# Performance work log

Hardware: AMD Instinct MI355X
Metric: run time of the kernel (lower is better)

The kernel has to match this reference:

```python
import jax, jax.numpy as jnp
import numpy as np

B, S, D, H = 2, 2048, 1024, 16
DK = D // H


def setup_inputs() -> dict:
    key = jax.random.key(0)
    ks = jax.random.split(key, 11)
    scale = 1.0 / np.sqrt(D)
    inp = {
        "k": jax.random.normal(ks[0], (B, S, D), jnp.float32),
        "q": jax.random.normal(ks[1], (B, S, D), jnp.float32),
        "v": jax.random.normal(ks[2], (B, S, D), jnp.float32),
        "w_q": jax.random.normal(ks[3], (D, D), jnp.float32) * scale,
        "b_q": jax.random.normal(ks[4], (D,), jnp.float32) * 0.01,
        "w_k": jax.random.normal(ks[5], (D, D), jnp.float32) * scale,
        "b_k": jax.random.normal(ks[6], (D,), jnp.float32) * 0.01,
        "w_v": jax.random.normal(ks[7], (D, D), jnp.float32) * scale,
        "b_v": jax.random.normal(ks[8], (D,), jnp.float32) * 0.01,
        "w_o": jax.random.normal(ks[9], (D, D), jnp.float32) * scale,
        "b_o": jax.random.normal(ks[10], (D,), jnp.float32) * 0.01,
        # causal mask; positions with mask==0 get -1e9 (masked_fill semantics)
        "mask": jnp.tril(jnp.ones((1, 1, S, S), jnp.int32)),
    }
    return inp


def reference(k, q, v, w_q, b_q, w_k, b_k, w_v, b_v, w_o, b_o, mask):
    MINUS_INF = -1000000000.0

    def proj(x, w, b):
        # nn.Linear: x @ w.T + b, then split heads -> [B, H, S, DK]
        y = x @ w.T + b
        return y.reshape(B, S, H, DK).transpose(0, 2, 1, 3)

    Q = proj(q, w_q, b_q)
    K = proj(k, w_k, b_k)
    V = proj(v, w_v, b_v)

    # [B, H, Sq, Sk] scores
    scores = jnp.einsum("bhqd,bhkd->bhqk", Q, K) / jnp.sqrt(jnp.float32(DK))
    scores = jnp.where(mask == 0, MINUS_INF, scores)
    attn = jax.nn.softmax(scores, axis=-1)

    out = jnp.einsum("bhqk,bhkd->bhqd", attn, V)  # [B, H, S, DK]
    out = out.transpose(0, 2, 1, 3).reshape(B, S, D)  # concat heads
    return out @ w_o.T + b_o
```

## Files before the change

kernel.cpp:

```cpp
#include <hip/hip_runtime.h>

typedef __bf16 bf16;
typedef __bf16 v8bf __attribute__((ext_vector_type(8)));
typedef __bf16 v4bf __attribute__((ext_vector_type(4)));
typedef float  v4f  __attribute__((ext_vector_type(4)));

#define MFMA16(a,b,c) __builtin_amdgcn_mfma_f32_16x16x32_bf16((a),(b),(c),0,0,0)

static constexpr int Sq = 2048;
static constexpr size_t NI = 4194304;
static constexpr size_t NW = 1048576;

__device__ __forceinline__ void gld_lds16(const void* g, void* l) {
  __builtin_amdgcn_global_load_lds(
      (__attribute__((address_space(1))) unsigned int*)g,
      (__attribute__((address_space(3))) unsigned int*)l,
      16, 0, 0);
}

__device__ __forceinline__ float exp2_raw(float x) {
  return __builtin_amdgcn_exp2f(x);
}

__global__ __launch_bounds__(256) void convert_kernel(
    const float* __restrict__ q, const float* __restrict__ k, const float* __restrict__ v,
    const float* __restrict__ wq, const float* __restrict__ wk,
    const float* __restrict__ wv, const float* __restrict__ wo,
    bf16* __restrict__ dst)
{
  const int NI4 = 1048576;
  const int NW4 = 262144;
  int idx = blockIdx.x * 256 + threadIdx.x;
  const float* src; size_t dstoff; int local;
  if (idx < 3 * NI4) {
    int a = idx >> 20; local = idx & (NI4 - 1);
    src = (a == 0) ? q : ((a == 1) ? k : v);
    dstoff = (size_t)a * NI;
  } else {
    int t = idx - 3 * NI4;
    int a = t >> 18; local = t & (NW4 - 1);
    src = (a == 0) ? wq : ((a == 1) ? wk : ((a == 2) ? wv : wo));
    dstoff = 3 * NI + (size_t)a * NW;
  }
  float4 f = ((const float4*)src)[local];
  v4bf hv = { (bf16)f.x, (bf16)f.y, (bf16)f.z, (bf16)f.w };
  *(v4bf*)(dst + dstoff + (size_t)local * 4) = hv;
}

__device__ __forceinline__ void gemm_bt_body(
    const bf16* __restrict__ A, const bf16* __restrict__ Bw,
    const float* __restrict__ bias, bf16* __restrict__ outh,
    float* __restrict__ outf, int bm, int bn, int mode)
{
  __shared__ alignas(16) bf16 As[128 * 32];
  __shared__ alignas(16) bf16 Bs[128 * 32];
  const int tid = threadIdx.x;
  const int wave = tid >> 6, lane = tid & 63;
  const int quad = lane >> 4, l15 = lane & 15;
  const int wm = (wave >> 1) * 64, wn = (wave & 1) * 64;
  const int lrow = lane >> 2, lcol = (lane & 3) * 8;

  v4f acc[4][4];
#pragma unroll
  for (int i = 0; i < 4; i++)
#pragma unroll
    for (int j = 0; j < 4; j++) { v4f z = {0.f, 0.f, 0.f, 0.f}; acc[i][j] = z; }

  const bf16* gA = A  + (size_t)(bm + wave * 32 + lrow) * 1024 + lcol;
  const bf16* gB = Bw + (size_t)(bn + wave * 32 + lrow) * 1024 + lcol;
  bf16* lA0 = &As[(wave * 32) * 32];
  bf16* lA1 = &As[(wave * 32 + 16) * 32];
  bf16* lB0 = &Bs[(wave * 32) * 32];
  bf16* lB1 = &Bs[(wave * 32 + 16) * 32];

  for (int k0 = 0; k0 < 1024; k0 += 32) {
    gld_lds16(gA + k0, lA0);
    gld_lds16(gA + 16 * 1024 + k0, lA1);
    gld_lds16(gB + k0, lB0);
    gld_lds16(gB + 16 * 1024 + k0, lB1);
    __syncthreads();
    v8bf af[4], bfr[4];
#pragma unroll
    for (int i = 0; i < 4; i++)
      af[i] = *(const v8bf*)&As[(wm + i * 16 + l15) * 32 + quad * 8];
#pragma unroll
    for (int j = 0; j < 4; j++)
      bfr[j] = *(const v8bf*)&Bs[(wn + j * 16 + l15) * 32 + quad * 8];
#pragma unroll
    for (int i = 0; i < 4; i++)
#pragma unroll
      for (int j = 0; j < 4; j++)
        acc[i][j] = MFMA16(af[i], bfr[j], acc[i][j]);
    __syncthreads();
  }

#pragma unroll
  for (int i = 0; i < 4; i++) {
    const int m0 = bm + wm + i * 16 + quad * 4;
#pragma unroll
    for (int j = 0; j < 4; j++) {
      const int n = bn + wn + j * 16 + l15;
      const float bv = bias[n];
      if (mode == 1) {
#pragma unroll
        for (int r = 0; r < 4; r++)
          outf[(size_t)(m0 + r) * 1024 + n] = acc[i][j][r] + bv;
      } else if (mode == 2) {
        int b_ = m0 >> 11, s_ = m0 & 2047;
        int h_ = n >> 6,  dk = n & 63;
        v4bf pk;
#pragma unroll
        for (int r = 0; r < 4; r++) pk[r] = (bf16)(acc[i][j][r] + bv);
        *(v4bf*)&outh[((size_t)((b_ * 16 + h_) * 64 + dk)) * 2048 + s_] = pk;
      } else {
        const float sc = (mode == 3) ? 0.18033688011112042f : 1.0f;
        int h_ = n >> 6,  dk = n & 63;
#pragma unroll
        for (int r = 0; r < 4; r++) {
          int m = m0 + r;
          int b_ = m >> 11, s_ = m & 2047;
          outh[(((size_t)(b_ * 16 + h_) * 2048 + s_) << 6) + dk] =
              (bf16)((acc[i][j][r] + bv) * sc);
        }
      }
    }
  }
}

__global__ __launch_bounds__(256, 2) void gemm_proj_kernel(
    const bf16* qb, const bf16* kb, const bf16* vb,
    const bf16* wqb, const bf16* wkb, const bf16* wvb,
    const float* bq, const float* bk, const float* bv,
    bf16* Qh, bf16* Kh, bf16* VhT)
{
  const bf16* A; const bf16* W; const float* bias; bf16* out; int mode;
  if (blockIdx.z == 0)      { A = qb; W = wqb; bias = bq; out = Qh;  mode = 3; }
  else if (blockIdx.z == 1) { A = kb; W = wkb; bias = bk; out = Kh;  mode = 0; }
  else                      { A = vb; W = wvb; bias = bv; out = VhT; mode = 2; }
  gemm_bt_body(A, W, bias, out, nullptr, blockIdx.y * 128, blockIdx.x * 128, mode);
}

__global__ __launch_bounds__(256, 2) void gemm_final_kernel(
    const bf16* Ob, const bf16* wob, const float* bo, float* out)
{
  gemm_bt_body(Ob, wob, bo, nullptr, out, blockIdx.y * 128, blockIdx.x * 128, 1);
}

__global__ __launch_bounds__(128, 2) void attn_kernel(
    const bf16* __restrict__ Qh, const bf16* __restrict__ Kh,
    const bf16* __restrict__ VhT, bf16* __restrict__ Ob)
{
  __shared__ alignas(16) bf16 Ps[2][32 * 72];
  const int tid = threadIdx.x;
  const int wave = tid >> 6, lane = tid & 63;
  const int quad = lane >> 4, l15 = lane & 15;
  const int bh = blockIdx.x, gy = blockIdx.y;
  const int b = bh >> 4, h = bh & 15;
  const int r8 = gy & 7, q8 = gy >> 3;
  const int u = 8 * q8 + ((q8 & 1) ? (7 - r8) : r8);
  const int qt = 2 * u + wave;
  const int L = u;
  const bf16* Qb = Qh + (size_t)bh * Sq * 64;
  const bf16* Kb = Kh + (size_t)bh * Sq * 64;
  const bf16* Vb = VhT + (size_t)bh * 64 * Sq;
  bf16* Pw = &Ps[wave][0];
  const int r0 = qt * 32;

  v8bf aq[2][2];
#pragma unroll
  for (int s = 0; s < 2; s++)
#pragma unroll
    for (int ks = 0; ks < 2; ks++)
      aq[s][ks] = *(const v8bf*)&Qb[(size_t)(r0 + s * 16 + l15) * 64 + ks * 32 + quad * 8];

  float lsum[2][4];
  v4f o[2][4];
#pragma unroll
  for (int s = 0; s < 2; s++)
#pragma unroll
    for (int r = 0; r < 4; r++) lsum[s][r] = 0.f;
#pragma unroll
  for (int s = 0; s < 2; s++)
#pragma unroll
    for (int j = 0; j < 4; j++) { v4f z = {0.f, 0.f, 0.f, 0.f}; o[s][j] = z; }

  auto loadK = [&](int kb, v8bf (&BK)[4][2]) {
#pragma unroll
    for (int n = 0; n < 4; n++) {
      BK[n][0] = *(const v8bf*)&Kb[(size_t)(kb + n * 16 + l15) * 64 + quad * 8];
      BK[n][1] = *(const v8bf*)&Kb[(size_t)(kb + n * 16 + l15) * 64 + 32 + quad * 8];
    }
  };
  auto loadV = [&](int kb, v8bf (&BV)[4][2]) {
#pragma unroll
    for (int n = 0; n < 4; n++) {
      BV[n][0] = *(const v8bf*)&Vb[(size_t)(n * 16 + l15) * 2048 + kb + quad * 8];
      BV[n][1] = *(const v8bf*)&Vb[(size_t)(n * 16 + l15) * 2048 + kb + 32 + quad * 8];
    }
  };
  auto compute = [&](const v8bf (&BK)[4][2], const v8bf (&BV)[4][2], int kc, bool diag) {
    const int kbase = kc * 64;
#pragma unroll
    for (int s = 0; s < 2; s++) {
      v4f cn[4];
#pragma unroll
      for (int n = 0; n < 4; n++) {
        v4f z = {0.f, 0.f, 0.f, 0.f};
        cn[n] = MFMA16(aq[s][0], BK[n][0], z);
        cn[n] = MFMA16(aq[s][1], BK[n][1], cn[n]);
      }
      const int rbase = r0 + s * 16 + quad * 4;
#pragma unroll
      for (int n = 0; n < 4; n++) {
        const int colg = kbase + n * 16 + l15;
#pragma unroll
        for (int r = 0; r < 4; r++) {
          float e = exp2_raw(cn[n][r]);
          if (diag && colg > rbase + r) e = 0.f;
          lsum[s][r] += e;
          Pw[(s * 16 + quad * 4 + r) * 72 + n * 16 + l15] = (bf16)e;
        }
      }
    }
#pragma unroll
    for (int s = 0; s < 2; s++) {
      v8bf ap0 = *(const v8bf*)&Pw[(s * 16 + l15) * 72 + quad * 8];
      v8bf ap1 = *(const v8bf*)&Pw[(s * 16 + l15) * 72 + 32 + quad * 8];
#pragma unroll
      for (int j = 0; j < 4; j++) {
        o[s][j] = MFMA16(ap0, BV[j][0], o[s][j]);
        o[s][j] = MFMA16(ap1, BV[j][1], o[s][j]);
      }
    }
  };

  v8bf bk0[4][2], bk1[4][2], bvv[4][2];
  loadK(0, bk0);
  int kc = 0;
  while (kc < L) {
    loadV(kc * 64, bvv);
    loadK((kc + 1) * 64, bk1);
    compute(bk0, bvv, kc, false);
    ++kc;
    if (kc >= L) {
      loadV(kc * 64, bvv);
      compute(bk1, bvv, kc, true);
      kc = -1;
      break;
    }
    loadV(kc * 64, bvv);
    loadK((kc + 1) * 64, bk0);
    compute(bk1, bvv, kc, false);
    ++kc;
  }
  if (kc >= 0) {
    loadV(kc * 64, bvv);
    compute(bk0, bvv, kc, true);
  }

#pragma unroll
  for (int s = 0; s < 2; s++)
#pragma unroll
    for (int r = 0; r < 4; r++) {
#pragma unroll
      for (int off = 1; off < 16; off <<= 1)
        lsum[s][r] += __shfl_xor(lsum[s][r], off, 64);
    }
#pragma unroll
  for (int s = 0; s < 2; s++)
#pragma unroll
    for (int r = 0; r < 4; r++) {
      const float inv = 1.0f / lsum[s][r];
      const int sg = r0 + s * 16 + quad * 4 + r;
#pragma unroll
      for (int j = 0; j < 4; j++)
        Ob[((size_t)(b * Sq + sg)) * 1024 + h * 64 + j * 16 + l15] =
            (bf16)(o[s][j][r] * inv);
    }
}

extern "C" void kernel_launch(void* const* d_in, const int* in_sizes, int n_in,
                              void* d_out, int out_size, void* d_ws, size_t ws_size,
                              hipStream_t stream) {
  (void)in_sizes; (void)n_in; (void)out_size; (void)ws_size;
  const float* kin = (const float*)d_in[0];
  const float* qin = (const float*)d_in[1];
  const float* vin = (const float*)d_in[2];
  const float* wq  = (const float*)d_in[3];
  const float* bq  = (const float*)d_in[4];
  const float* wk  = (const float*)d_in[5];
  const float* bk  = (const float*)d_in[6];
  const float* wv  = (const float*)d_in[7];
  const float* bv  = (const float*)d_in[8];
  const float* wo  = (const float*)d_in[9];
  const float* bo  = (const float*)d_in[10];

  bf16* ws = (bf16*)d_ws;
  bf16* qb  = ws;
  bf16* kb  = ws + NI;
  bf16* vb  = ws + 2 * NI;
  bf16* wqb = ws + 3 * NI;
  bf16* wkb = wqb + NW;
  bf16* wvb = wqb + 2 * NW;
  bf16* wob = wqb + 3 * NW;
  bf16* Qh  = ws + 3 * NI + 4 * NW;
  bf16* Kh  = Qh + NI;
  bf16* VhT = Qh + 2 * NI;
  bf16* Ob  = Qh + 3 * NI;

  convert_kernel<<<16384, 256, 0, stream>>>(qin, kin, vin, wq, wk, wv, wo, ws);
  gemm_proj_kernel<<<dim3(8, 32, 3), 256, 0, stream>>>(
      qb, kb, vb, wqb, wkb, wvb, bq, bk, bv, Qh, Kh, VhT);
  attn_kernel<<<dim3(32, 32), 128, 0, stream>>>(Qh, Kh, VhT, Ob);
  gemm_final_kernel<<<dim3(8, 32), 256, 0, stream>>>(Ob, wob, bo, (float*)d_out);
}
```

Before: 261.4 us.

## Split attention key range across two wave pairs and merge partials in LDS

Each attention block now runs four waves: two waves per query tile split the causal key-block range in half, and the second half writes its unnormalized output and row sums to shared memory for the first half to combine. This relies on the softmax using a fixed (non-running) max so partial sums add directly. The aim is more parallelism and shorter serial key loops per block, especially for long causal rows. The cost is extra LDS traffic, a block-wide barrier, higher LDS use per block, and imbalance when the split is uneven for small u.

Result: slower. 419.4 us (+60.5%).

```diff
diff --git a/kernel.cpp b/kernel.cpp
--- a/kernel.cpp
+++ b/kernel.cpp
@@ -146,11 +146,13 @@
   gemm_bt_body(Ob, wob, bo, nullptr, out, blockIdx.y * 128, blockIdx.x * 128, 1);
 }
 
-__global__ __launch_bounds__(128, 2) void attn_kernel(
+__global__ __launch_bounds__(256, 4) void attn_kernel(
     const bf16* __restrict__ Qh, const bf16* __restrict__ Kh,
     const bf16* __restrict__ VhT, bf16* __restrict__ Ob)
 {
-  __shared__ alignas(16) bf16 Ps[2][32 * 72];
+  __shared__ alignas(16) bf16 Ps[4][32 * 72];
+  __shared__ alignas(16) float Osum[2][32][66];
+  __shared__ float Lsum[2][32];
   const int tid = threadIdx.x;
   const int wave = tid >> 6, lane = tid & 63;
   const int quad = lane >> 4, l15 = lane & 15;
@@ -158,8 +160,12 @@
   const int b = bh >> 4, h = bh & 15;
   const int r8 = gy & 7, q8 = gy >> 3;
   const int u = 8 * q8 + ((q8 & 1) ? (7 - r8) : r8);
-  const int qt = 2 * u + wave;
-  const int L = u;
+  const int tw = wave & 1;
+  const int half = wave >> 1;
+  const int qt = 2 * u + tw;
+  const int m = (u + 2) >> 1;
+  const int lo = half ? m : 0;
+  const int hi = half ? u : (m - 1);
   const bf16* Qb = Qh + (size_t)bh * Sq * 64;
   const bf16* Kb = Kh + (size_t)bh * Sq * 64;
   const bf16* Vb = VhT + (size_t)bh * 64 * Sq;
@@ -234,28 +240,30 @@
     }
   };
 
-  v8bf bk0[4][2], bk1[4][2], bvv[4][2];
-  loadK(0, bk0);
-  int kc = 0;
-  while (kc < L) {
-    loadV(kc * 64, bvv);
-    loadK((kc + 1) * 64, bk1);
-    compute(bk0, bvv, kc, false);
-    ++kc;
-    if (kc >= L) {
+  if (lo <= hi) {
+    v8bf bk0[4][2], bk1[4][2], bvv[4][2];
+    loadK(lo * 64, bk0);
+    int kc = lo;
+    while (kc < hi) {
       loadV(kc * 64, bvv);
-      compute(bk1, bvv, kc, true);
-      kc = -1;
-      break;
-    }
-    loadV(kc * 64, bvv);
-    loadK((kc + 1) * 64, bk0);
-    compute(bk1, bvv, kc, false);
-    ++kc;
-  }
-  if (kc >= 0) {
-    loadV(kc * 64, bvv);
-    compute(bk0, bvv, kc, true);
+      loadK((kc + 1) * 64, bk1);
+      compute(bk0, bvv, kc, false);
+      ++kc;
+      if (kc >= hi) {
+        loadV(kc * 64, bvv);
+        compute(bk1, bvv, kc, kc == u);
+        kc = -1;
+        break;
+      }
+      loadV(kc * 64, bvv);
+      loadK((kc + 1) * 64, bk0);
+      compute(bk1, bvv, kc, false);
+      ++kc;
+    }
+    if (kc >= 0) {
+      loadV(kc * 64, bvv);
+      compute(bk0, bvv, kc, kc == u);
+    }
   }
 
 #pragma unroll
@@ -266,17 +274,38 @@
       for (int off = 1; off < 16; off <<= 1)
         lsum[s][r] += __shfl_xor(lsum[s][r], off, 64);
     }
-#pragma unroll
-  for (int s = 0; s < 2; s++)
-#pragma unroll
-    for (int r = 0; r < 4; r++) {
-      const float inv = 1.0f / lsum[s][r];
-      const int sg = r0 + s * 16 + quad * 4 + r;
+
+  if (half == 1) {
+#pragma unroll
+    for (int s = 0; s < 2; s++)
 #pragma unroll
       for (int j = 0; j < 4; j++)
-        Ob[((size_t)(b * Sq + sg)) * 1024 + h * 64 + j * 16 + l15] =
-            (bf16)(o[s][j][r] * inv);
-    }
+#pragma unroll
+        for (int r = 0; r < 4; r++)
+          Osum[tw][s * 16 + quad * 4 + r][j * 16 + l15] = o[s][j][r];
+    if (l15 == 0) {
+#pragma unroll
+      for (int s = 0; s < 2; s++)
+#pragma unroll
+        for (int r = 0; r < 4; r++)
+          Lsum[tw][s * 16 + quad * 4 + r] = lsum[s][r];
+    }
+  }
+  __syncthreads();
+  if (half == 0) {
+#pragma unroll
+    for (int s = 0; s < 2; s++)
+#pragma unroll
+      for (int r = 0; r < 4; r++) {
+        const int row = s * 16 + quad * 4 + r;
+        const float inv = 1.0f / (lsum[s][r] + Lsum[tw][row]);
+        const int sg = r0 + row;
+#pragma unroll
+        for (int j = 0; j < 4; j++)
+          Ob[((size_t)(b * Sq + sg)) * 1024 + h * 64 + j * 16 + l15] =
+              (bf16)((o[s][j][r] + Osum[tw][row][j * 16 + l15]) * inv);
+      }
+  }
 }
 
 extern "C" void kernel_launch(void* const* d_in, const int* in_sizes, int n_in,
@@ -311,6 +340,6 @@
   convert_kernel<<<16384, 256, 0, stream>>>(qin, kin, vin, wq, wk, wv, wo, ws);
   gemm_proj_kernel<<<dim3(8, 32, 3), 256, 0, stream>>>(
       qb, kb, vb, wqb, wkb, wvb, bq, bk, bv, Qh, Kh, VhT);
-  attn_kernel<<<dim3(32, 32), 128, 0, stream>>>(Qh, Kh, VhT, Ob);
+  attn_kernel<<<dim3(32, 32), 256, 0, stream>>>(Qh, Kh, VhT, Ob);
   gemm_final_kernel<<<dim3(8, 32), 256, 0, stream>>>(Ob, wob, bo, (float*)d_out);
 }
```
